# Kernel optimization log

Measured on AMD Instinct MI355X. Metric: run time of the kernel, lower is better.

The kernel has to match this reference:

```python
import jax, jax.numpy as jnp
import numpy as np

NUM_EMBEDDINGS = 512
EMBEDDING_DIM = 64
DECAY = 0.995
EXPECTED_COUNT = 1024 * 16 * 16 / NUM_EMBEDDINGS  # batch_size * H * W / K = 512.0


def setup_inputs() -> dict:
    key = jax.random.key(0)
    k1, k2 = jax.random.split(key)
    z_e = jax.random.normal(k1, (1024, EMBEDDING_DIM, 16, 16), dtype=jnp.float32)
    e = jax.random.normal(k2, (NUM_EMBEDDINGS, EMBEDDING_DIM), dtype=jnp.float32)
    N = jnp.ones((NUM_EMBEDDINGS,), dtype=jnp.float32) * EXPECTED_COUNT
    return {"z_e": z_e, "e": e, "N": N}


def reference(z_e, e, N):
    B, D, H, W = z_e.shape
    # (B, D, H, W) -> (B*H*W, D)
    z_flat = jnp.transpose(z_e, (0, 2, 3, 1)).reshape(-1, D)
    # squared euclidean distances: ||z||^2 + ||e||^2 - 2 z.e^T  -> [B*H*W, K]
    dist = (
        jnp.sum(z_flat * z_flat, axis=1, keepdims=True)
        + jnp.sum(e * e, axis=1)[None, :]
        - 2.0 * (z_flat @ e.T)
    )
    indices_flat = jnp.argmin(dist, axis=1)
    # embedding gather, back to (B, D, H, W)
    z_q = e[indices_flat].reshape(B, H, W, D)
    z_q = jnp.transpose(z_q, (0, 3, 1, 2))
    # training-mode EMA bincount update of cluster counts
    n_i = jnp.zeros((e.shape[0],), dtype=jnp.float32).at[indices_flat].add(1.0)
    N_new = DECAY * N + (1.0 - DECAY) * n_i
    return z_q, N_new
```

## Files before the change

### kernel.cpp

```cpp
#include <hip/hip_runtime.h>

#define KCODES 512
#define DIM    64
#define PXB    512
#define NCT    32
#define MARGIN 0.125f

typedef __attribute__((ext_vector_type(8))) short    short8;
typedef __attribute__((ext_vector_type(8))) _Float16 half8;
typedef __attribute__((ext_vector_type(4))) float    floatx4;

__global__ __launch_bounds__(256) void vq_setup(const float* __restrict__ e,
        float* __restrict__ enorm, _Float16* __restrict__ ehf,
        float* __restrict__ counts, unsigned* __restrict__ tick)
{
    const int tg = blockIdx.x * 256 + threadIdx.x;
    const int c = tg >> 6, j = tg & 63;
    const int p = j >> 3, i = j & 7;
    const int dsrc = ((p ^ (c & 7)) << 3) | i;
    ehf[tg] = (_Float16)(-2.f * e[c * DIM + dsrc]);
    if (tg < KCODES) {
        const float* er = e + tg * DIM;
        float s = 0.f;
        #pragma unroll
        for (int d = 0; d < DIM; ++d) s = fmaf(er[d], er[d], s);
        enorm[tg]  = s;
        counts[tg] = 0.f;
        if (tg == 0) *tick = 0u;
    }
}

__global__ __launch_bounds__(1024, 8) void vq_main(
        const float* __restrict__ z, const float* __restrict__ e,
        const _Float16* __restrict__ ehf, const float* __restrict__ enorm,
        const float* __restrict__ N, float* __restrict__ zq,
        float* __restrict__ counts, unsigned* __restrict__ tick,
        float* __restrict__ outN)
{
    __shared__ __align__(16) _Float16 eHs[KCODES * DIM];
    __shared__ float ens[KCODES];
    __shared__ int   hist[KCODES];
    __shared__ int   idxs[PXB];
    __shared__ int   ref2[PXB];
    __shared__ int   lastflag;

    const int t    = threadIdx.x;
    const int b    = blockIdx.x;
    const int lane = t & 63;
    const int wave = t >> 6;
    const int n16  = lane & 15;
    const int g4   = lane >> 4;

    {
        const short8* src = (const short8*)ehf;
        short8* dst = (short8*)eHs;
        #pragma unroll
        for (int k = 0; k < 4; ++k)
            dst[t + k * 1024] = src[t + k * 1024];
        if (t < KCODES) { ens[t] = enorm[t]; hist[t] = 0; }
    }

    const int gp0 = b * PXB + wave * 32;
    half8 A[2][2];
    #pragma unroll
    for (int pt = 0; pt < 2; ++pt) {
        const int gp = gp0 + pt * 16 + n16;
        const int bb = gp >> 8, hw = gp & 255;
        const float* zb = z + (size_t)bb * (DIM * 256) + hw;
        #pragma unroll
        for (int ks = 0; ks < 2; ++ks) {
            float v[8];
            #pragma unroll
            for (int q = 0; q < 8; ++q)
                v[q] = zb[(size_t)(ks * 32 + g4 * 8 + q) * 256];
            half8 h;
            #pragma unroll
            for (int q = 0; q < 8; ++q) h[q] = (_Float16)v[q];
            A[pt][ks] = h;
        }
    }

    __syncthreads();

    const int xr = n16 & 7;
    const int byte0 = n16 * 128 + (((g4    ) ^ xr) << 4);
    const int byte1 = n16 * 128 + (((4 | g4) ^ xr) << 4);
    const char* hb = (const char*)eHs;

    float bestv[2][4];
    int   bct[2][4];
    #pragma unroll
    for (int pt = 0; pt < 2; ++pt)
        #pragma unroll
        for (int r = 0; r < 4; ++r) { bestv[pt][r] = 3.4e38f; bct[pt][r] = 0; }

    #pragma unroll 2
    for (int ct = 0; ct < NCT; ++ct) {
        const int cb = ct * 2048;
        half8 B0 = *(const half8*)(hb + cb + byte0);
        half8 B1 = *(const half8*)(hb + cb + byte1);
        const float en = ens[ct * 16 + n16];
        #pragma unroll
        for (int pt = 0; pt < 2; ++pt) {
            floatx4 C = {en, en, en, en};
            C = __builtin_amdgcn_mfma_f32_16x16x32_f16(A[pt][0], B0, C, 0, 0, 0);
            C = __builtin_amdgcn_mfma_f32_16x16x32_f16(A[pt][1], B1, C, 0, 0, 0);
            #pragma unroll
            for (int r = 0; r < 4; ++r) {
                float s = C[r];
                if (s < bestv[pt][r]) { bestv[pt][r] = s; bct[pt][r] = ct; }
            }
        }
    }

    #pragma unroll
    for (int pt = 0; pt < 2; ++pt)
        #pragma unroll
        for (int r = 0; r < 4; ++r) {
            const float v1 = bestv[pt][r];
            const int   i1 = bct[pt][r] * 16 + n16;
            float v = v1; int i = i1;
            #pragma unroll
            for (int off = 1; off < 16; off <<= 1) {
                float vs = __shfl_xor(v, off, 16);
                int   is = __shfl_xor(i, off, 16);
                if (vs < v || (vs == v && is < i)) { v = vs; i = is; }
            }
            float w  = (i1 == i) ? 3.4e38f : v1;
            int   wi = i1;
            #pragma unroll
            for (int off = 1; off < 16; off <<= 1) {
                float vs = __shfl_xor(w, off, 16);
                int   is = __shfl_xor(wi, off, 16);
                if (vs < w || (vs == w && is < wi)) { w = vs; wi = is; }
            }
            if (n16 == 0) {
                const int px = wave * 32 + pt * 16 + g4 * 4 + r;
                idxs[px] = i;
                ref2[px] = (w - v < MARGIN) ? wi : -1;
            }
        }

    __syncthreads();

    if (t < PXB) {
        int bi = idxs[t];
        const int r2 = ref2[t];
        if (r2 >= 0) {
            const int gp = b * PXB + t;
            const int bb = gp >> 8, hw = gp & 255;
            const float* zb = z + (size_t)bb * (DIM * 256) + hw;
            const float* e1 = e + bi * DIM;
            const float* e2 = e + r2 * DIM;
            float d1 = 0.f, d2 = 0.f;
            #pragma unroll
            for (int d = 0; d < DIM; ++d) {
                const float zd = zb[(size_t)d * 256];
                d1 = fmaf(zd, e1[d], d1);
                d2 = fmaf(zd, e2[d], d2);
            }
            const float s1 = fmaf(-2.f, d1, ens[bi]);
            const float s2 = fmaf(-2.f, d2, ens[r2]);
            if (s2 < s1 || (s2 == s1 && r2 < bi)) bi = r2;
            idxs[t] = bi;
        }
        atomicAdd(&hist[bi], 1);
    }

    __syncthreads();

    if (t < KCODES) { int h = hist[t]; if (h) atomicAdd(&counts[t], (float)h); }
    __syncthreads();
    if (t == 0) {
        __threadfence();
        unsigned o = __hip_atomic_fetch_add(tick, 1u, __ATOMIC_ACQ_REL,
                                            __HIP_MEMORY_SCOPE_AGENT);
        lastflag = (o == gridDim.x - 1u);
    }
    __syncthreads();

    {
        const int px = t & 511, dh = (t >> 9) * 32;
        const int bi = idxs[px];
        const int gp = b * PXB + px;
        const int bb = gp >> 8, hw = gp & 255;
        const float4* er4 = (const float4*)(e + bi * DIM + dh);
        float* ob = zq + (size_t)bb * (DIM * 256) + (size_t)dh * 256 + hw;
        #pragma unroll
        for (int q = 0; q < 8; ++q) {
            float4 v = er4[q];
            ob[(size_t)(4 * q + 0) * 256] = v.x;
            ob[(size_t)(4 * q + 1) * 256] = v.y;
            ob[(size_t)(4 * q + 2) * 256] = v.z;
            ob[(size_t)(4 * q + 3) * 256] = v.w;
        }
    }

    if (lastflag && t < KCODES) {
        float c = __hip_atomic_load(&counts[t], __ATOMIC_RELAXED,
                                    __HIP_MEMORY_SCOPE_AGENT);
        outN[t] = 0.995f * N[t] + 0.005f * c;
    }
}

extern "C" void kernel_launch(void* const* d_in, const int* in_sizes, int n_in,
                              void* d_out, int out_size, void* d_ws, size_t ws_size,
                              hipStream_t stream) {
    const float* z = (const float*)d_in[0];
    const float* e = (const float*)d_in[1];
    const float* N = (const float*)d_in[2];
    float* out = (float*)d_out;
    const int nz     = in_sizes[0];
    const int npix   = nz / DIM;
    const int blocks = npix / PXB;

    char* ws = (char*)d_ws;
    float*     enorm  = (float*)(ws);
    float*     counts = (float*)(ws + 2048);
    unsigned*  tick   = (unsigned*)(ws + 4096);
    _Float16*  ehf    = (_Float16*)(ws + 4352);

    vq_setup<<<(KCODES * DIM) / 256, 256, 0, stream>>>(e, enorm, ehf, counts, tick);
    vq_main<<<blocks, 1024, 0, stream>>>(z, e, ehf, enorm, N, out, counts,
                                         tick, out + nz);
}
```

Before: 171.7 us.

## Stage z through LDS with vectorized loads and transpose reads; DPP top-2 merge

Loads the block's z tile with coalesced float4 global loads, converts to fp16 into shared memory, then builds MFMA A-fragments via ds_read_b64_tr_b16 transpose reads instead of strided scalar global loads. The codebook layout is permuted (sigma_dim) to match the new A-fragment dimension ordering. The top-2 argmin reduction is replaced by packed 64-bit monotonic keys merged with DPP row operations instead of shuffles. This adds two extra barriers and reuses the shared buffer for z then codebook.

```diff
diff --git a/kernel.cpp b/kernel.cpp
--- a/kernel.cpp
+++ b/kernel.cpp
@@ -6,9 +6,14 @@
 #define NCT    32
 #define MARGIN 0.125f
 
-typedef __attribute__((ext_vector_type(8))) short    short8;
-typedef __attribute__((ext_vector_type(8))) _Float16 half8;
-typedef __attribute__((ext_vector_type(4))) float    floatx4;
+typedef __attribute__((ext_vector_type(8))) short        short8;
+typedef __attribute__((ext_vector_type(8))) _Float16     half8;
+typedef __attribute__((ext_vector_type(4))) float        floatx4;
+typedef __attribute__((ext_vector_type(2))) unsigned int uint2v;
+
+__device__ __host__ inline int sigma_dim(int p) {
+    return ((p >> 5) << 5) + (((p >> 2) & 1) << 4) + (((p >> 3) & 3) << 2) + (p & 3);
+}
 
 __global__ __launch_bounds__(256) void vq_setup(const float* __restrict__ e,
         float* __restrict__ enorm, _Float16* __restrict__ ehf,
@@ -16,8 +21,9 @@
 {
     const int tg = blockIdx.x * 256 + threadIdx.x;
     const int c = tg >> 6, j = tg & 63;
-    const int p = j >> 3, i = j & 7;
-    const int dsrc = ((p ^ (c & 7)) << 3) | i;
+    const int g = j >> 3, i = j & 7;
+    const int gs = g ^ (c & 7);
+    const int dsrc = sigma_dim(gs * 8 + i);
     ehf[tg] = (_Float16)(-2.f * e[c * DIM + dsrc]);
     if (tg < KCODES) {
         const float* er = e + tg * DIM;
@@ -29,6 +35,28 @@
         if (tg == 0) *tick = 0u;
     }
 }
+
+__device__ inline unsigned mono(float f) {
+    unsigned u = __float_as_uint(f);
+    return (u & 0x80000000u) ? ~u : (u | 0x80000000u);
+}
+__device__ inline float unmono(unsigned u) {
+    return __uint_as_float((u & 0x80000000u) ? (u & 0x7FFFFFFFu) : ~u);
+}
+
+#define DPP64(dst, src, CTRL) {                                                       \
+    int _lo = __builtin_amdgcn_update_dpp(0, (int)(unsigned)((src) & 0xFFFFFFFFull),  \
+                                          CTRL, 0xF, 0xF, true);                      \
+    int _hi = __builtin_amdgcn_update_dpp(0, (int)(unsigned)((src) >> 32),            \
+                                          CTRL, 0xF, 0xF, true);                      \
+    dst = (((unsigned long long)(unsigned)_hi) << 32) | (unsigned)_lo; }
+
+#define MERGE_STEP(CTRL) {                                                            \
+    unsigned long long o1, o2; DPP64(o1, k1, CTRL); DPP64(o2, k2, CTRL);              \
+    unsigned long long mx  = k1 > o1 ? k1 : o1;                                       \
+    unsigned long long mn2 = k2 < o2 ? k2 : o2;                                       \
+    k1 = k1 < o1 ? k1 : o1;                                                           \
+    k2 = mx < mn2 ? mx : mn2; }
 
 __global__ __launch_bounds__(1024, 8) void vq_main(
         const float* __restrict__ z, const float* __restrict__ e,
@@ -37,7 +65,7 @@
         float* __restrict__ counts, unsigned* __restrict__ tick,
         float* __restrict__ outN)
 {
-    __shared__ __align__(16) _Float16 eHs[KCODES * DIM];
+    __shared__ __align__(16) _Float16 S[KCODES * DIM];
     __shared__ float ens[KCODES];
     __shared__ int   hist[KCODES];
     __shared__ int   idxs[PXB];
@@ -51,41 +79,70 @@
     const int n16  = lane & 15;
     const int g4   = lane >> 4;
 
+    if (t < KCODES) { ens[t] = enorm[t]; hist[t] = 0; }
+
+    {
+        float4 v[8];
+        #pragma unroll
+        for (int i = 0; i < 8; ++i) {
+            const int L  = i * 1024 + t;
+            const int bb = L >> 12, d = (L >> 6) & 63, c4 = L & 63;
+            v[i] = *(const float4*)(z + (size_t)((b * 2 + bb) * DIM + d) * 256 + c4 * 4);
+        }
+        #pragma unroll
+        for (int i = 0; i < 8; ++i) {
+            const int L  = i * 1024 + t;
+            const int bb = L >> 12, d = (L >> 6) & 63, c4 = L & 63;
+            union { _Float16 h[4]; uint2v u; } pk;
+            pk.h[0] = (_Float16)v[i].x; pk.h[1] = (_Float16)v[i].y;
+            pk.h[2] = (_Float16)v[i].z; pk.h[3] = (_Float16)v[i].w;
+            const int chunk = bb * 16 + (c4 >> 2);
+            *(uint2v*)(S + chunk * 1024 + d * 16 + (c4 & 3) * 4) = pk.u;
+        }
+    }
+    __syncthreads();
+
+    half8 A[2][2];
+    {
+        uint2v r[2][2][2];
+        const int trb = n16 * 2 + g4 * 128;
+        #pragma unroll
+        for (int pt = 0; pt < 2; ++pt) {
+            const int base = (wave * 2 + pt) * 2048 + trb;
+            #pragma unroll
+            for (int ks = 0; ks < 2; ++ks) {
+                const int a0 = base + ks * 1024;
+                asm volatile("ds_read_b64_tr_b16 %0, %1" : "=v"(r[pt][ks][0]) : "v"(a0));
+                asm volatile("ds_read_b64_tr_b16 %0, %1" : "=v"(r[pt][ks][1]) : "v"(a0 + 512));
+            }
+        }
+        asm volatile("s_waitcnt lgkmcnt(0)" ::: "memory");
+        __builtin_amdgcn_sched_barrier(0);
+        #pragma unroll
+        for (int pt = 0; pt < 2; ++pt)
+            #pragma unroll
+            for (int ks = 0; ks < 2; ++ks) {
+                union { unsigned int u[4]; half8 h; } pk;
+                pk.u[0] = r[pt][ks][0].x; pk.u[1] = r[pt][ks][0].y;
+                pk.u[2] = r[pt][ks][1].x; pk.u[3] = r[pt][ks][1].y;
+                A[pt][ks] = pk.h;
+            }
+    }
+    __syncthreads();
+
     {
         const short8* src = (const short8*)ehf;
-        short8* dst = (short8*)eHs;
+        short8* dst = (short8*)S;
         #pragma unroll
         for (int k = 0; k < 4; ++k)
             dst[t + k * 1024] = src[t + k * 1024];
-        if (t < KCODES) { ens[t] = enorm[t]; hist[t] = 0; }
-    }
-
-    const int gp0 = b * PXB + wave * 32;
-    half8 A[2][2];
-    #pragma unroll
-    for (int pt = 0; pt < 2; ++pt) {
-        const int gp = gp0 + pt * 16 + n16;
-        const int bb = gp >> 8, hw = gp & 255;
-        const float* zb = z + (size_t)bb * (DIM * 256) + hw;
-        #pragma unroll
-        for (int ks = 0; ks < 2; ++ks) {
-            float v[8];
-            #pragma unroll
-            for (int q = 0; q < 8; ++q)
-                v[q] = zb[(size_t)(ks * 32 + g4 * 8 + q) * 256];
-            half8 h;
-            #pragma unroll
-            for (int q = 0; q < 8; ++q) h[q] = (_Float16)v[q];
-            A[pt][ks] = h;
-        }
-    }
-
+    }
     __syncthreads();
 
     const int xr = n16 & 7;
     const int byte0 = n16 * 128 + (((g4    ) ^ xr) << 4);
     const int byte1 = n16 * 128 + (((4 | g4) ^ xr) << 4);
-    const char* hb = (const char*)eHs;
+    const char* hb = (const char*)S;
 
     float bestv[2][4];
     int   bct[2][4];
@@ -117,27 +174,20 @@
     for (int pt = 0; pt < 2; ++pt)
         #pragma unroll
         for (int r = 0; r < 4; ++r) {
-            const float v1 = bestv[pt][r];
-            const int   i1 = bct[pt][r] * 16 + n16;
-            float v = v1; int i = i1;
-            #pragma unroll
-            for (int off = 1; off < 16; off <<= 1) {
-                float vs = __shfl_xor(v, off, 16);
-                int   is = __shfl_xor(i, off, 16);
-                if (vs < v || (vs == v && is < i)) { v = vs; i = is; }
-            }
-            float w  = (i1 == i) ? 3.4e38f : v1;
-            int   wi = i1;
-            #pragma unroll
-            for (int off = 1; off < 16; off <<= 1) {
-                float vs = __shfl_xor(w, off, 16);
-                int   is = __shfl_xor(wi, off, 16);
-                if (vs < w || (vs == w && is < wi)) { w = vs; wi = is; }
-            }
+            unsigned long long k1 =
+                (((unsigned long long)mono(bestv[pt][r])) << 32)
+                | (unsigned)(bct[pt][r] * 16 + n16);
+            unsigned long long k2 = ~0ull;
+            MERGE_STEP(0xB1);
+            MERGE_STEP(0x4E);
+            MERGE_STEP(0x124);
+            MERGE_STEP(0x128);
             if (n16 == 0) {
                 const int px = wave * 32 + pt * 16 + g4 * 4 + r;
-                idxs[px] = i;
-                ref2[px] = (w - v < MARGIN) ? wi : -1;
+                const float f1 = unmono((unsigned)(k1 >> 32));
+                const float f2 = unmono((unsigned)(k2 >> 32));
+                idxs[px] = (int)(k1 & 0xFFFFFFFFull);
+                ref2[px] = (f2 - f1 < MARGIN) ? (int)(k2 & 0xFFFFFFFFull) : -1;
             }
         }
 
@@ -166,7 +216,6 @@
         }
         atomicAdd(&hist[bi], 1);
     }
-
     __syncthreads();
 
     if (t < KCODES) { int h = hist[t]; if (h) atomicAdd(&counts[t], (float)h); }
```

Result: faster. 167.7 us (-2.3%).
